# Optimization experiments

Hardware: AMD Instinct MI355X
Metric: run time of the kernel (lower is better)

## Reference

```python
import jax, jax.numpy as jnp
import numpy as np

HIDDEN = 1024
HEADS = 16
HEAD_DIM = HIDDEN // HEADS


def setup_inputs() -> dict:
    key = jax.random.key(0)
    ks = jax.random.split(key, 11)
    B, S = 2, 2048
    s = 1.0 / np.sqrt(HIDDEN)
    return {
        "query": jax.random.normal(ks[0], (B, S, HIDDEN), jnp.float32),
        "key": jax.random.normal(ks[1], (B, S, HIDDEN), jnp.float32),
        "value": jax.random.normal(ks[2], (B, S, HIDDEN), jnp.float32),
        "Wq": jax.random.uniform(ks[3], (HIDDEN, HIDDEN), jnp.float32, -s, s),
        "bq": jax.random.uniform(ks[4], (HIDDEN,), jnp.float32, -s, s),
        "Wk": jax.random.uniform(ks[5], (HIDDEN, HIDDEN), jnp.float32, -s, s),
        "bk": jax.random.uniform(ks[6], (HIDDEN,), jnp.float32, -s, s),
        "Wv": jax.random.uniform(ks[7], (HIDDEN, HIDDEN), jnp.float32, -s, s),
        "bv": jax.random.uniform(ks[8], (HIDDEN,), jnp.float32, -s, s),
        "Wo": jax.random.uniform(ks[9], (HIDDEN, HIDDEN), jnp.float32, -s, s),
        "bo": jax.random.uniform(ks[10], (HIDDEN,), jnp.float32, -s, s),
    }


def reference(query, key, value, Wq, bq, Wk, bk, Wv, bv, Wo, bo):
    B, Sq, _ = query.shape
    Sk = key.shape[1]
    # projections (torch Linear: x @ W^T + b)
    Q = (query @ Wq.T + bq).reshape(B, Sq, HEADS, HEAD_DIM).transpose(0, 2, 1, 3)
    K = (key @ Wk.T + bk).reshape(B, Sk, HEADS, HEAD_DIM).transpose(0, 2, 1, 3)
    V = (value @ Wv.T + bv).reshape(B, Sk, HEADS, HEAD_DIM).transpose(0, 2, 1, 3)
    scale = jnp.sqrt(jnp.float32(HEAD_DIM))
    scores = jnp.einsum("bhqd,bhkd->bhqk", Q, K) / scale  # [B,H,Sq,Sk]
    # causal mask (is_causal=True, Sq>1)
    causal = jnp.tril(jnp.ones((Sq, Sk), dtype=bool))
    scores = jnp.where(causal[None, None], scores, -jnp.inf)
    attn = jax.nn.softmax(scores, axis=-1)
    out = jnp.einsum("bhqk,bhkd->bhqd", attn, V)
    out = out.transpose(0, 2, 1, 3).reshape(B, Sq, HIDDEN)
    return out @ Wo.T + bo
```

## Files before the change

### kernel.cpp

```cpp
#include <hip/hip_runtime.h>
#include <hip/hip_bf16.h>


typedef __attribute__((ext_vector_type(4)))  float f32x4;
typedef __attribute__((ext_vector_type(16))) float f32x16;
typedef __attribute__((ext_vector_type(8)))  short bf16x8;
typedef unsigned short u16;

#define SEQ   2048
#define NH    16
#define HD    64
#define HID   1024
#define CEXP  0.1803368801f
#define MEG   1048576u
#define MASKV (-30000.0f)

#define BAR()    __builtin_amdgcn_s_barrier()
#define SCHED0() __builtin_amdgcn_sched_barrier(0)

static __device__ __forceinline__ u16 f2bf(float f) {
  union { __hip_bfloat16 h; u16 u; } c;
  c.h = __float2bfloat16(f);
  return c.u;
}

static __device__ __forceinline__ int swz(int row, int col8) {
  return col8 ^ ((row & 7) << 3);
}

static __device__ __forceinline__ void gll16(const void* g, void* l) {
  __builtin_amdgcn_global_load_lds(
      (const __attribute__((address_space(1))) void*)g,
      (__attribute__((address_space(3))) void*)l, 16, 0, 0);
}

__global__ __launch_bounds__(256) void cvt_kernel(
    const float* __restrict__ Wq, const float* __restrict__ Wk,
    const float* __restrict__ Wv, const float* __restrict__ Wo,
    const float* __restrict__ q, const float* __restrict__ k,
    const float* __restrict__ v,
    u16* __restrict__ wsout, u16* __restrict__ dob) {
  const int y = blockIdx.y;
  const int c = y & 3;
  const float* src;
  u16* dst;
  if (y < 4) {
    src = (y == 0) ? Wq : (y == 1) ? Wk : (y == 2) ? Wv : Wo;
    dst = wsout + (size_t)y * MEG;
  } else if (y < 8) {
    src = q + (size_t)c * MEG;
    dst = wsout + 4u * MEG + (size_t)c * MEG;
  } else if (y < 12) {
    src = k + (size_t)c * MEG;
    dst = dob + (size_t)c * MEG;
  } else {
    src = v + (size_t)c * MEG;
    dst = dob + 4u * MEG + (size_t)c * MEG;
  }
  int i = (blockIdx.x * 256 + threadIdx.x) * 4;
  float4 f = *(const float4*)(src + i);
  ushort4 o;
  o.x = f2bf(f.x); o.y = f2bf(f.y); o.z = f2bf(f.z); o.w = f2bf(f.w);
  *(ushort4*)(dst + i) = o;
}

__global__ __launch_bounds__(256) void proj_kernel(
    const u16* __restrict__ Xq, const u16* __restrict__ Xk,
    const u16* __restrict__ Xv, const u16* __restrict__ Wc,
    const float* __restrict__ bq, const float* __restrict__ bk,
    const float* __restrict__ bvp,
    u16* __restrict__ Qo, u16* __restrict__ Ko, u16* __restrict__ Vto) {
  __shared__ u16 As[2][128 * 64];
  __shared__ u16 Bs[2][64 * 64];

  const int tid  = threadIdx.x;
  const int lane = tid & 63;
  const int wid  = tid >> 6;
  const int wm   = wid >> 1, wn = wid & 1;
  const int l15  = lane & 15;
  const int lhi  = lane >> 4;
  const int z    = blockIdx.z;
  const int bm   = blockIdx.x * 128;
  const int bn   = blockIdx.y * 64;

  const u16* X = (z == 0) ? Xq : (z == 1) ? Xk : Xv;
  const u16* W = Wc + (size_t)z * (HID * HID);
  const float* bias = (z == 0) ? bq : (z == 1) ? bk : bvp;

  f32x4 acc[4][2];
#pragma unroll
  for (int i = 0; i < 4; i++)
#pragma unroll
    for (int j = 0; j < 2; j++) acc[i][j] = (f32x4){0.f, 0.f, 0.f, 0.f};

  const int lrow  = lane >> 3;
  const int gcol8 = lane & 7;

#define PROJ_STAGE(buf, k0)                                                       \
  {                                                                               \
    _Pragma("unroll")                                                             \
    for (int c = 0; c < 4; c++) {                                                 \
      const int row  = c * 32 + wid * 8 + lrow;                                   \
      const int scol = (gcol8 ^ (row & 7)) * 8;      \
      gll16(X + (size_t)(bm + row) * HID + (k0) + scol,                           \
            (char*)&As[buf][0] + c * 4096 + wid * 1024);                          \
      if (c < 2)                                                                  \
        gll16(W + (size_t)(bn + row) * HID + (k0) + scol,                         \
              (char*)&Bs[buf][0] + c * 4096 + wid * 1024);                        \
    }                                                                             \
  }

  PROJ_STAGE(0, 0);
  for (int t = 0; t < 16; t++) {
    BAR();
    if (t < 15) {
      PROJ_STAGE((t + 1) & 1, (t + 1) * 64);
      asm volatile("s_waitcnt vmcnt(6)" ::: "memory");
    } else {
      asm volatile("s_waitcnt vmcnt(0)" ::: "memory");
    }
    BAR();
    SCHED0();
    const u16* A = &As[t & 1][0];
    const u16* B = &Bs[t & 1][0];
#pragma unroll
    for (int ks = 0; ks < 2; ks++) {
      bf16x8 af[4], bfm[2];
#pragma unroll
      for (int i = 0; i < 4; i++) {
        const int row = wm * 64 + i * 16 + l15;
        af[i] = *(const bf16x8*)&A[row * 64 + swz(row, ks * 32 + lhi * 8)];
      }
#pragma unroll
      for (int j = 0; j < 2; j++) {
        const int row = wn * 32 + j * 16 + l15;
        bfm[j] = *(const bf16x8*)&B[row * 64 + swz(row, ks * 32 + lhi * 8)];
      }
#pragma unroll
      for (int i = 0; i < 4; i++)
#pragma unroll
        for (int j = 0; j < 2; j++)
          acc[i][j] = __builtin_amdgcn_mfma_f32_16x16x32_bf16(af[i], bfm[j], acc[i][j], 0, 0, 0);
    }
  }
#undef PROJ_STAGE

  const int bb = bm >> 11;
#pragma unroll
  for (int j = 0; j < 2; j++) {
    const int n = bn + wn * 32 + j * 16 + l15;
    const float bv_ = bias[n];
    const int h = n >> 6, d = n & 63;
    if (z == 2) {
#pragma unroll
      for (int i = 0; i < 4; i++) {
        const int s0 = (bm + wm * 64 + i * 16 + lhi * 4) & 2047;
        ushort4 t;
        t.x = f2bf(acc[i][j][0] + bv_);
        t.y = f2bf(acc[i][j][1] + bv_);
        t.z = f2bf(acc[i][j][2] + bv_);
        t.w = f2bf(acc[i][j][3] + bv_);
        *(ushort4*)&Vto[((size_t)(bb * NH + h) * HD + d) * SEQ + s0] = t;
      }
    } else {
      u16* O = z ? Ko : Qo;
#pragma unroll
      for (int i = 0; i < 4; i++)
#pragma unroll
        for (int r = 0; r < 4; r++) {
          const int m = bm + wm * 64 + i * 16 + lhi * 4 + r;
          const int s = m & 2047;
          O[(((size_t)(bb * NH + h) * SEQ + s) << 6) + d] = f2bf(acc[i][j][r] + bv_);
        }
    }
  }
}

__global__ __launch_bounds__(512) void attn_kernel(
    const u16* __restrict__ Q, const u16* __restrict__ K,
    const u16* __restrict__ Vt, u16* __restrict__ Aout) {
  __shared__ __align__(16) char pool[36864];

  const int tid  = threadIdx.x;
  const int lane = tid & 63;
  const int wid  = tid >> 6;
  const int wq   = wid & 3;
  const int g    = wid >> 2;
  const int l31  = lane & 31;
  const int gp   = lane >> 5;

  const int flat = blockIdx.x;
  const int slot = flat >> 3;
  const int bh   = (flat & 7) * 4 + (slot & 3);
  const int qt   = 15 - (slot >> 2);
  const int b    = bh >> 4, h = bh & 15;
  const size_t base = (size_t)bh * SEQ * HD;

  const int qrow = qt * 128 + wq * 32 + l31;
  const int qmax = qt * 128 + wq * 32 + 31;
  bf16x8 aq[4];
#pragma unroll
  for (int ds = 0; ds < 4; ds++)
    aq[ds] = *(const bf16x8*)&Q[base + (size_t)qrow * HD + ds * 16 + gp * 8];

  f32x16 o[2];
#pragma unroll
  for (int r = 0; r < 16; r++) { o[0][r] = 0.f; o[1][r] = 0.f; }
  float m_s = -1e30f, l_s = 0.f;

  const int st   = tid & 255;
  const int gs   = tid >> 8;
  const int srow = st >> 2;
  const int sd   = (st & 3) * 16;
  const int kc0  = sd >> 3;
  u16* Ks_s = (u16*)(pool + gs * 16384);
  u16* Vs_s = (u16*)(pool + gs * 16384 + 8192);
  const int kwz0 = srow * 64 + ((kc0       ^ (srow & 7)) << 3);
  const int kwz1 = srow * 64 + (((kc0 + 1) ^ (srow & 7)) << 3);

  union B2S { bf16x8 v; short4 s[2]; };
  B2S pk0, pk1, pv0, pv1;

#define LOADR(kt_)                                                                \
  {                                                                               \
    const u16* kp = K + base + (size_t)((kt_) * 64 + srow) * HD + sd;             \
    pk0.v = *(const bf16x8*)kp;                                                   \
    pk1.v = *(const bf16x8*)(kp + 8);                                             \
    const u16* vp = Vt + base + (size_t)srow * SEQ + (kt_) * 64 + sd;             \
    pv0.v = *(const bf16x8*)vp;                                                   \
    pv1.v = *(const bf16x8*)(vp + 8);                                             \
  }

  LOADR(gs);

  const int nit = qt + 1;
  for (int it = 0; it < nit; ++it) {
    BAR();
    *(bf16x8*)&Ks_s[kwz0] = pk0.v;
    *(bf16x8*)&Ks_s[kwz1] = pk1.v;
    *(short4*)&Vs_s[kwz0]     = pv0.s[0];
    *(short4*)&Vs_s[kwz0 + 4] = pv1.s[0];
    *(short4*)&Vs_s[kwz1]     = pv0.s[1];
    *(short4*)&Vs_s[kwz1 + 4] = pv1.s[1];
    if (it + 1 < nit) LOADR(2 * (it + 1) + gs);
    asm volatile("s_waitcnt lgkmcnt(0)" ::: "memory");
    BAR();
    SCHED0();

    const int kt = 2 * it + g;
    const bool act = (kt * 64) <= qmax;
    if (act) {
      const u16* Ksh = (const u16*)(pool + g * 16384);
      const u16* Vsh = (const u16*)(pool + g * 16384 + 8192);

      f32x16 sc[2];
      __builtin_amdgcn_s_setprio(1);
#pragma unroll
      for (int kb = 0; kb < 2; kb++) {
#pragma unroll
        for (int r = 0; r < 16; r++) sc[kb][r] = 0.f;
#pragma unroll
        for (int ds = 0; ds < 4; ds++) {
          const int row = kb * 32 + l31;
          bf16x8 kf = *(const bf16x8*)&Ksh[row * 64 + (((2 * ds + gp) ^ (row & 7)) << 3)];
          sc[kb] = __builtin_amdgcn_mfma_f32_32x32x16_bf16(kf, aq[ds], sc[kb], 0, 0, 0);
        }
      }
      __builtin_amdgcn_s_setprio(0);

      if (kt >= 2 * qt) {
#pragma unroll
        for (int kb = 0; kb < 2; kb++)
#pragma unroll
          for (int r = 0; r < 16; r++) {
            const int kg = kt * 64 + kb * 32 + (r & 3) + 8 * (r >> 2) + 4 * gp;
            if (kg > qrow) sc[kb][r] = MASKV;
          }
      }

      float mx = -1e30f;
#pragma unroll
      for (int kb = 0; kb < 2; kb++)
#pragma unroll
        for (int r = 0; r < 16; r++) mx = fmaxf(mx, sc[kb][r]);
      mx = fmaxf(mx, __shfl_xor(mx, 32, 64));
      if (__any(mx > m_s + 64.0f)) {
        const float mnew = fmaxf(m_s, mx);
        const float fac = __builtin_amdgcn_exp2f((m_s - mnew) * CEXP);
        l_s *= fac;
        m_s = mnew;
        float facr[16];
#pragma unroll
        for (int r = 0; r < 16; r++)
          facr[r] = __shfl(fac, (r & 3) + 8 * (r >> 2) + 4 * gp, 64);
#pragma unroll
        for (int r = 0; r < 16; r++) { o[0][r] *= facr[r]; o[1][r] *= facr[r]; }
      }
      const float nmc = -m_s * CEXP;
      float ps = 0.f;
#pragma unroll
      for (int kb = 0; kb < 2; kb++)
#pragma unroll
        for (int r = 0; r < 16; r++) {
          const float e = __builtin_amdgcn_exp2f(fmaf(sc[kb][r], CEXP, nmc));
          sc[kb][r] = e;
          ps += e;
        }
      ps += __shfl_xor(ps, 32, 64);
      l_s += ps;

      __builtin_amdgcn_s_setprio(1);
#pragma unroll
      for (int kb = 0; kb < 2; kb++)
#pragma unroll
        for (int ss = 0; ss < 2; ss++) {
          bf16x8 pa;
#pragma unroll
          for (int j = 0; j < 8; j++) pa[j] = (short)f2bf(sc[kb][ss * 8 + j]);
          const int chunk = (kb * 2 + ss) * 2 + gp;
#pragma unroll
          for (int dt = 0; dt < 2; dt++) {
            const int row = dt * 32 + l31;
            bf16x8 bv = *(const bf16x8*)&Vsh[row * 64 + ((chunk ^ (row & 7)) << 3)];
            o[dt] = __builtin_amdgcn_mfma_f32_32x32x16_bf16(pa, bv, o[dt], 0, 0, 0);
          }
        }
      __builtin_amdgcn_s_setprio(0);
    }
  }
#undef LOADR

  BAR();
  f32x4* comb = (f32x4*)pool;
  const int ci = (wq * 64 + lane) * 9;
  if (g == 0) {
#pragma unroll
    for (int dt = 0; dt < 2; dt++)
#pragma unroll
      for (int qq = 0; qq < 4; qq++)
        comb[ci + dt * 4 + qq] =
            (f32x4){o[dt][qq * 4 + 0], o[dt][qq * 4 + 1],
                    o[dt][qq * 4 + 2], o[dt][qq * 4 + 3]};
    comb[ci + 8] = (f32x4){m_s, l_s, 0.f, 0.f};
  }
  BAR();
  if (g == 1) {
    f32x4 ml = comb[ci + 8];
    const float m0 = ml[0], l0 = ml[1];
    const float M  = fmaxf(m0, m_s);
    float u0 = __builtin_amdgcn_exp2f((m0 - M) * CEXP);
    float u1 = __builtin_amdgcn_exp2f((m_s - M) * CEXP);
    const float inv = 1.0f / (l0 * u0 + l_s * u1);
    u0 *= inv; u1 *= inv;
    float u0r[16], u1r[16];
#pragma unroll
    for (int r = 0; r < 16; r++) {
      const int mapr = (r & 3) + 8 * (r >> 2) + 4 * gp;
      u0r[r] = __shfl(u0, mapr, 64);
      u1r[r] = __shfl(u1, mapr, 64);
    }
#pragma unroll
    for (int dt = 0; dt < 2; dt++)
#pragma unroll
      for (int r = 0; r < 16; r++) {
        const float o0v = comb[ci + dt * 4 + (r >> 2)][r & 3];
        const float val = o0v * u0r[r] + o[dt][r] * u1r[r];
        const int rowg = qt * 128 + wq * 32 + (r & 3) + 8 * (r >> 2) + 4 * gp;
        Aout[(((size_t)(b * SEQ + rowg)) << 10) + h * 64 + dt * 32 + l31] = f2bf(val);
      }
  }
}

__global__ __launch_bounds__(256) void oproj_kernel(
    const u16* __restrict__ X, const u16* __restrict__ W,
    const float* __restrict__ bias, float* __restrict__ Out) {
  __shared__ u16 As[2][128 * 64];
  __shared__ u16 Bs[2][64 * 64];

  const int tid  = threadIdx.x;
  const int lane = tid & 63;
  const int wid  = tid >> 6;
  const int wm   = wid >> 1, wn = wid & 1;
  const int l15  = lane & 15;
  const int lhi  = lane >> 4;
  const int bm   = blockIdx.x * 128;
  const int bn   = blockIdx.y * 64;

  f32x4 acc[4][2];
#pragma unroll
  for (int i = 0; i < 4; i++)
#pragma unroll
    for (int j = 0; j < 2; j++) acc[i][j] = (f32x4){0.f, 0.f, 0.f, 0.f};

  const int lrow  = lane >> 3;
  const int gcol8 = lane & 7;

#define OPROJ_STAGE(buf, k0)                                                      \
  {                                                                               \
    _Pragma("unroll")                                                             \
    for (int c = 0; c < 4; c++) {                                                 \
      const int row  = c * 32 + wid * 8 + lrow;                                   \
      const int scol = (gcol8 ^ (row & 7)) * 8;                                   \
      gll16(X + (size_t)(bm + row) * HID + (k0) + scol,                           \
            (char*)&As[buf][0] + c * 4096 + wid * 1024);                          \
      if (c < 2)                                                                  \
        gll16(W + (size_t)(bn + row) * HID + (k0) + scol,                         \
              (char*)&Bs[buf][0] + c * 4096 + wid * 1024);                        \
    }                                                                             \
  }

  OPROJ_STAGE(0, 0);
  for (int t = 0; t < 16; t++) {
    BAR();
    if (t < 15) {
      OPROJ_STAGE((t + 1) & 1, (t + 1) * 64);
      asm volatile("s_waitcnt vmcnt(6)" ::: "memory");
    } else {
      asm volatile("s_waitcnt vmcnt(0)" ::: "memory");
    }
    BAR();
    SCHED0();
    const u16* A = &As[t & 1][0];
    const u16* B = &Bs[t & 1][0];
#pragma unroll
    for (int ks = 0; ks < 2; ks++) {
      bf16x8 af[4], bfm[2];
#pragma unroll
      for (int i = 0; i < 4; i++) {
        const int row = wm * 64 + i * 16 + l15;
        af[i] = *(const bf16x8*)&A[row * 64 + swz(row, ks * 32 + lhi * 8)];
      }
#pragma unroll
      for (int j = 0; j < 2; j++) {
        const int row = wn * 32 + j * 16 + l15;
        bfm[j] = *(const bf16x8*)&B[row * 64 + swz(row, ks * 32 + lhi * 8)];
      }
#pragma unroll
      for (int i = 0; i < 4; i++)
#pragma unroll
        for (int j = 0; j < 2; j++)
          acc[i][j] = __builtin_amdgcn_mfma_f32_16x16x32_bf16(af[i], bfm[j], acc[i][j], 0, 0, 0);
    }
  }
#undef OPROJ_STAGE

#pragma unroll
  for (int j = 0; j < 2; j++) {
    const int n = bn + wn * 32 + j * 16 + l15;
    const float bv_ = bias[n];
#pragma unroll
    for (int i = 0; i < 4; i++)
#pragma unroll
      for (int r = 0; r < 4; r++) {
        const int m = bm + wm * 64 + i * 16 + lhi * 4 + r;
        Out[(size_t)m * HID + n] = acc[i][j][r] + bv_;
      }
  }
}

extern "C" void kernel_launch(void* const* d_in, const int* in_sizes, int n_in,
                              void* d_out, int out_size, void* d_ws, size_t ws_size,
                              hipStream_t stream) {
  const float* q  = (const float*)d_in[0];
  const float* k  = (const float*)d_in[1];
  const float* v  = (const float*)d_in[2];
  const float* Wq = (const float*)d_in[3];
  const float* bq = (const float*)d_in[4];
  const float* Wk = (const float*)d_in[5];
  const float* bk = (const float*)d_in[6];
  const float* Wv = (const float*)d_in[7];
  const float* bv = (const float*)d_in[8];
  const float* Wo = (const float*)d_in[9];
  const float* bo = (const float*)d_in[10];

  u16* ws   = (u16*)d_ws;
  u16* wqkv = ws;
  u16* wob  = ws + 3u * MEG;
  u16* qb   = ws + 4u * MEG;
  u16* Qb   = ws + 8u * MEG;
  u16* Kb   = ws + 12u * MEG;
  u16* Vtb  = ws + 16u * MEG;
  u16* Ab   = qb;
  u16* kbf  = (u16*)d_out;
  u16* vbf  = (u16*)d_out + 4u * MEG;

  cvt_kernel<<<dim3(1024, 16), 256, 0, stream>>>(Wq, Wk, Wv, Wo, q, k, v, ws, kbf);

  proj_kernel<<<dim3(32, 16, 3), 256, 0, stream>>>(qb, kbf, vbf, wqkv, bq, bk, bv,
                                                   Qb, Kb, Vtb);

  attn_kernel<<<dim3(512), 512, 0, stream>>>(Qb, Kb, Vtb, Ab);

  oproj_kernel<<<dim3(32, 16), 256, 0, stream>>>(Ab, wob, bo, (float*)d_out);
}
```

Baseline: 99.22 us.

## Double-buffer attention K/V LDS tiles and change swizzle pattern

The attention kernel now keeps two LDS buffers per group for K and V tiles, writing the next tile while the current one is consumed, and issues global loads two iterations ahead. This leaves one barrier per iteration instead of two and hides global load latency behind the MFMA work. The swizzle is also changed to a row+row/8 based XOR, and the V stores are merged into full 16-byte writes. LDS use grows from 36KB to 64KB per block, which may reduce occupancy.

```diff
diff --git a/kernel.cpp b/kernel.cpp
--- a/kernel.cpp
+++ b/kernel.cpp
@@ -26,6 +26,10 @@
 
 static __device__ __forceinline__ int swz(int row, int col8) {
   return col8 ^ ((row & 7) << 3);
+}
+
+static __device__ __forceinline__ int s8k(int row) {
+  return (row + (row >> 3)) & 7;
 }
 
 static __device__ __forceinline__ void gll16(const void* g, void* l) {
@@ -179,7 +183,7 @@
 __global__ __launch_bounds__(512) void attn_kernel(
     const u16* __restrict__ Q, const u16* __restrict__ K,
     const u16* __restrict__ Vt, u16* __restrict__ Aout) {
-  __shared__ __align__(16) char pool[36864];
+  __shared__ __align__(16) char pool[65536];
 
   const int tid  = threadIdx.x;
   const int lane = tid & 63;
@@ -213,10 +217,9 @@
   const int srow = st >> 2;
   const int sd   = (st & 3) * 16;
   const int kc0  = sd >> 3;
-  u16* Ks_s = (u16*)(pool + gs * 16384);
-  u16* Vs_s = (u16*)(pool + gs * 16384 + 8192);
-  const int kwz0 = srow * 64 + ((kc0       ^ (srow & 7)) << 3);
-  const int kwz1 = srow * 64 + (((kc0 + 1) ^ (srow & 7)) << 3);
+  const int sw   = s8k(srow);
+  const int kwz0 = srow * 64 + ((kc0       ^ sw) << 3);
+  const int kwz1 = srow * 64 + (((kc0 + 1) ^ sw) << 3);
 
   union B2S { bf16x8 v; short4 s[2]; };
   B2S pk0, pk1, pv0, pv1;
@@ -230,28 +233,36 @@
     pv0.v = *(const bf16x8*)vp;                                                   \
     pv1.v = *(const bf16x8*)(vp + 8);                                             \
   }
-
+#define WRITE_LDS(wb_)                                                            \
+  {                                                                               \
+    u16* Ks_ = (u16*)(pool + (gs * 2 + (wb_)) * 8192);                            \
+    u16* Vs_ = (u16*)(pool + 32768 + (gs * 2 + (wb_)) * 8192);                    \
+    *(bf16x8*)&Ks_[kwz0] = pk0.v;                                                 \
+    *(bf16x8*)&Ks_[kwz1] = pk1.v;                                                 \
+    B2S w0, w1;                                                                   \
+    w0.s[0] = pv0.s[0]; w0.s[1] = pv1.s[0];                                       \
+    w1.s[0] = pv0.s[1]; w1.s[1] = pv1.s[1];                                       \
+    *(bf16x8*)&Vs_[kwz0] = w0.v;                                                  \
+    *(bf16x8*)&Vs_[kwz1] = w1.v;                                                  \
+  }
+
+  const int nit = qt + 1;
   LOADR(gs);
-
-  const int nit = qt + 1;
+  WRITE_LDS(0);
+  asm volatile("s_waitcnt lgkmcnt(0)" ::: "memory");
+  BAR();
+  if (nit > 1) LOADR(2 + gs);
+
   for (int it = 0; it < nit; ++it) {
-    BAR();
-    *(bf16x8*)&Ks_s[kwz0] = pk0.v;
-    *(bf16x8*)&Ks_s[kwz1] = pk1.v;
-    *(short4*)&Vs_s[kwz0]     = pv0.s[0];
-    *(short4*)&Vs_s[kwz0 + 4] = pv1.s[0];
-    *(short4*)&Vs_s[kwz1]     = pv0.s[1];
-    *(short4*)&Vs_s[kwz1 + 4] = pv1.s[1];
-    if (it + 1 < nit) LOADR(2 * (it + 1) + gs);
-    asm volatile("s_waitcnt lgkmcnt(0)" ::: "memory");
-    BAR();
-    SCHED0();
+    const int cb = it & 1;
+    if (it + 1 < nit) WRITE_LDS((it + 1) & 1);
+    if (it + 2 < nit) LOADR(2 * (it + 2) + gs);
 
     const int kt = 2 * it + g;
     const bool act = (kt * 64) <= qmax;
     if (act) {
-      const u16* Ksh = (const u16*)(pool + g * 16384);
-      const u16* Vsh = (const u16*)(pool + g * 16384 + 8192);
+      const u16* Ksh = (const u16*)(pool + (g * 2 + cb) * 8192);
+      const u16* Vsh = (const u16*)(pool + 32768 + (g * 2 + cb) * 8192);
 
       f32x16 sc[2];
       __builtin_amdgcn_s_setprio(1);
@@ -262,7 +273,7 @@
 #pragma unroll
         for (int ds = 0; ds < 4; ds++) {
           const int row = kb * 32 + l31;
-          bf16x8 kf = *(const bf16x8*)&Ksh[row * 64 + (((2 * ds + gp) ^ (row & 7)) << 3)];
+          bf16x8 kf = *(const bf16x8*)&Ksh[row * 64 + (((2 * ds + gp) ^ s8k(row)) << 3)];
           sc[kb] = __builtin_amdgcn_mfma_f32_32x32x16_bf16(kf, aq[ds], sc[kb], 0, 0, 0);
         }
       }
@@ -321,16 +332,18 @@
 #pragma unroll
           for (int dt = 0; dt < 2; dt++) {
             const int row = dt * 32 + l31;
-            bf16x8 bv = *(const bf16x8*)&Vsh[row * 64 + ((chunk ^ (row & 7)) << 3)];
+            bf16x8 bv = *(const bf16x8*)&Vsh[row * 64 + ((chunk ^ s8k(row)) << 3)];
             o[dt] = __builtin_amdgcn_mfma_f32_32x32x16_bf16(pa, bv, o[dt], 0, 0, 0);
           }
         }
       __builtin_amdgcn_s_setprio(0);
     }
+    asm volatile("s_waitcnt lgkmcnt(0)" ::: "memory");
+    BAR();
   }
 #undef LOADR
-
-  BAR();
+#undef WRITE_LDS
+
   f32x4* comb = (f32x4*)pool;
   const int ci = (wq * 64 + lane) * 9;
   if (g == 0) {
```

After: 100.9 us. No clear change (+1.7%).
